# Kernel tuning notes

Hardware: AMD Instinct MI355X
Metric: run time of the kernel (lower is better)

## Reference

```python
import jax, jax.numpy as jnp
import numpy as np

N, MAX_SIZE, SPATIAL = 50000, 32, 27
CH_IN, CH_OUT = 128, 128


def setup_inputs() -> dict:
    key = jax.random.key(0)
    k1, k2, k3, k4 = jax.random.split(key, 4)
    feat_in = jax.random.normal(k1, (N, CH_IN), dtype=jnp.float32)
    select_mat = jax.random.uniform(k2, (N, MAX_SIZE, SPATIAL), dtype=jnp.float32)
    # kaiming-uniform-ish init for weight of shape [SPATIAL, CH_OUT*CH_IN]
    fan_in = CH_OUT * CH_IN
    bound = np.sqrt(6.0 / fan_in)
    weight = jax.random.uniform(k3, (SPATIAL, CH_OUT * CH_IN), dtype=jnp.float32,
                                minval=-bound, maxval=bound)
    neighbor_idx = jax.random.randint(k4, (N, MAX_SIZE), 0, N, dtype=jnp.int64)
    return {"feat_in": feat_in, "select_mat": select_mat,
            "weight": weight, "neighbor_idx": neighbor_idx}


def reference(feat_in, select_mat, weight, neighbor_idx):
    # feat_in: [N, I]; select_mat: [N, M, S]; weight: [S, O*I]; neighbor_idx: [N, M]
    ch_in = feat_in.shape[1]
    spatial = weight.shape[0]
    ch_out = weight.shape[1] // ch_in
    w = weight.reshape(spatial, ch_out, ch_in)          # [S, O, I]
    patch_feat = feat_in[neighbor_idx]                  # irregular gather -> [N, M, I]
    # Original math: out[n,o] = sum_m sum_s sel[n,m,s] * W[s,o,i] * pf[n,m,i]
    # Contract neighbor dim first to avoid the [N, M, O, I] intermediate.
    t = jnp.einsum('nms,nmi->nsi', select_mat, patch_feat)   # [N, S, I]
    feat_out = jnp.einsum('nsi,soi->no', t, w)               # [N, O]
    return feat_out[:, :, None]                              # [N, O, 1]
```

## Files before the change

### kernel.cpp

```cpp
#include <hip/hip_runtime.h>


#define N_CHI 128
#define N_SP  27
#define N_M   32
#define KDIM  (N_SP * N_CHI)
#define SEL_STRIDE (N_M * N_SP)

typedef short s16x8 __attribute__((ext_vector_type(8)));
typedef s16x8 __attribute__((may_alias)) s16x8_a;
typedef unsigned short u16x8 __attribute__((ext_vector_type(8)));
typedef u16x8 __attribute__((may_alias)) u16x8_a;
typedef unsigned short u16x4 __attribute__((ext_vector_type(4)));
typedef u16x4 __attribute__((may_alias)) u16x4_a;
typedef unsigned int u32x2 __attribute__((ext_vector_type(2)));
typedef u32x2 __attribute__((may_alias)) u32x2_a;
typedef float f32x4 __attribute__((ext_vector_type(4)));
typedef f32x4 __attribute__((may_alias)) f32x4_a;
typedef float f32x16 __attribute__((ext_vector_type(16)));

typedef __attribute__((address_space(3))) unsigned int as3_u32;
typedef __attribute__((address_space(1))) const unsigned int as1_u32;

static __device__ __forceinline__ unsigned short f2bf(float f) {
  unsigned int u = __float_as_uint(f);
  u += 0x7FFFu + ((u >> 16) & 1u);
  return (unsigned short)(u >> 16);
}

__global__ __launch_bounds__(128) void wconv_kernel(const float* __restrict__ w,
                                                    unsigned short* __restrict__ Wt) {
  const int s = blockIdx.x;
  const int o = blockIdx.y;
  const int i = threadIdx.x;
  Wt[((size_t)o * N_SP + s) * N_CHI + i] = f2bf(w[((size_t)s * 128 + o) * N_CHI + i]);
}

__global__ __launch_bounds__(256) void featconv_kernel(
    const float* __restrict__ feat, unsigned short* __restrict__ featb, int total4) {
  const int t = blockIdx.x * 256 + threadIdx.x;
  if (t < total4) {
    f32x4 v = ((const f32x4_a*)feat)[t];
    u16x4 o;
#pragma unroll
    for (int j = 0; j < 4; ++j) o[j] = f2bf(v[j]);
    ((u16x4_a*)featb)[t] = o;
  }
}

__global__ __launch_bounds__(256) void phase1_kernel(
    const unsigned short* __restrict__ featb, const float* __restrict__ sel,
    const int* __restrict__ nidx, unsigned short* __restrict__ T,
    int nbase, int nend) {
  __shared__ __align__(16) unsigned short selT[4][32 * 40];
  __shared__ __align__(16) unsigned short tbuf[4][N_SP * 128];
  const int wave = threadIdx.x >> 6;
  const int lane = threadIdx.x & 63;
  const int n = nbase + (int)blockIdx.x * 4 + wave;
  if (n >= nend) return;
  unsigned short* st = selT[wave];
  unsigned short* tb = tbuf[wave];

  const float* selp = sel + (size_t)n * SEL_STRIDE;
#pragma unroll
  for (int it = 0; it < 16; ++it) {
    int e = it * 64 + lane;
    int m = e >> 5, s = e & 31;
    float v = (s < N_SP) ? selp[m * N_SP + s] : 0.0f;
    st[s * 40 + m] = f2bf(v);
  }

  const int q = lane >> 5;
  const int col = lane & 31;

  const int* ip = nidx + (size_t)n * N_M;
  size_t roff[16];
#pragma unroll
  for (int ks = 0; ks < 2; ++ks)
#pragma unroll
    for (int j = 0; j < 8; ++j)
      roff[ks * 8 + j] = (size_t)ip[ks * 16 + q * 8 + j] << 7;

  const s16x8 bf0 = *(const s16x8_a*)&st[col * 40 + q * 8];
  const s16x8 bf1 = *(const s16x8_a*)&st[col * 40 + 16 + q * 8];

#pragma unroll
  for (int ti = 0; ti < 4; ++ti) {
    const int icol = ti * 32 + col;
    unsigned short fv[16];
#pragma unroll
    for (int t = 0; t < 16; ++t) fv[t] = featb[roff[t] + icol];
    s16x8 af0, af1;
#pragma unroll
    for (int j = 0; j < 8; ++j) {
      af0[j] = (short)fv[j];
      af1[j] = (short)fv[8 + j];
    }
    f32x16 acc = {0.f, 0.f, 0.f, 0.f, 0.f, 0.f, 0.f, 0.f,
                  0.f, 0.f, 0.f, 0.f, 0.f, 0.f, 0.f, 0.f};
    acc = __builtin_amdgcn_mfma_f32_32x32x16_bf16(af0, bf0, acc, 0, 0, 0);
    acc = __builtin_amdgcn_mfma_f32_32x32x16_bf16(af1, bf1, acc, 0, 0, 0);
    if (col < N_SP) {
#pragma unroll
      for (int g = 0; g < 4; ++g) {
        const int b16 = ti * 4 + g;
        const int phys16 = b16 ^ (col & 15);
        u32x2 pk;
        pk[0] = (unsigned int)f2bf(acc[4 * g + 0]) | ((unsigned int)f2bf(acc[4 * g + 1]) << 16);
        pk[1] = (unsigned int)f2bf(acc[4 * g + 2]) | ((unsigned int)f2bf(acc[4 * g + 3]) << 16);
        *(u32x2_a*)&tb[col * 128 + phys16 * 8 + q * 4] = pk;
      }
    }
  }

  unsigned short* Tn = T + (size_t)(n - nbase) * KDIM;
#pragma unroll
  for (int it = 0; it < 7; ++it) {
    const int P = it * 64 + lane;
    if (P < 432) {
      const int c = P >> 4;
      const int b16 = P & 15;
      const int phys16 = b16 ^ (c & 15);
      *(u16x8_a*)&Tn[(size_t)P * 8] = *(const u16x8_a*)&tb[c * 128 + phys16 * 8];
    }
  }
}

__global__ __launch_bounds__(256) void phase2_kernel(
    const unsigned short* __restrict__ T, const unsigned short* __restrict__ Wt,
    float* __restrict__ out, int nbase, int N) {
  __shared__ __align__(16) unsigned short Alds[64 * 128];
  __shared__ __align__(16) unsigned short Blds[128 * 128];
  const int tid = threadIdx.x;
  const int lane = tid & 63;
  const int wbase = tid & ~63;
  const int wave = tid >> 6;
  const int wm = wave & 1, wn = wave >> 1;
  const int quad = lane >> 4, l16 = lane & 15;
  const size_t rowbase = (size_t)blockIdx.x * 64;

  f32x4 acc[2][4];
#pragma unroll
  for (int a = 0; a < 2; ++a)
#pragma unroll
    for (int b = 0; b < 4; ++b) acc[a][b] = (f32x4){0.f, 0.f, 0.f, 0.f};

  const unsigned short* aga[4];
  const unsigned short* bga[8];
#pragma unroll
  for (int it = 0; it < 4; ++it) {
    const int slot = it * 256 + tid;
    const int r = slot >> 4, bp = slot & 15;
    aga[it] = T + (rowbase + r) * KDIM + ((bp ^ (r & 15)) << 3);
  }
#pragma unroll
  for (int it = 0; it < 8; ++it) {
    const int slot = it * 256 + tid;
    const int r = slot >> 4, bp = slot & 15;
    bga[it] = Wt + (size_t)r * KDIM + ((bp ^ (r & 15)) << 3);
  }

  for (int kt = 0; kt < KDIM / 128; ++kt) {
    const int k0 = kt * 128;
#pragma unroll
    for (int it = 0; it < 4; ++it)
      __builtin_amdgcn_global_load_lds(
          (as1_u32*)(const void*)(aga[it] + k0),
          (as3_u32*)(void*)&Alds[(it * 256 + wbase) * 8], 16, 0, 0);
#pragma unroll
    for (int it = 0; it < 8; ++it)
      __builtin_amdgcn_global_load_lds(
          (as1_u32*)(const void*)(bga[it] + k0),
          (as3_u32*)(void*)&Blds[(it * 256 + wbase) * 8], 16, 0, 0);
    __syncthreads();
#pragma unroll
    for (int ks = 0; ks < 4; ++ks) {
      const int bg = ks * 4 + quad;
      s16x8 af[2], bfr[4];
#pragma unroll
      for (int mt = 0; mt < 2; ++mt) {
        const int m = wm * 32 + mt * 16 + l16;
        af[mt] = *(const s16x8_a*)&Alds[m * 128 + ((bg ^ (m & 15)) << 3)];
      }
#pragma unroll
      for (int nt = 0; nt < 4; ++nt) {
        const int o = wn * 64 + nt * 16 + l16;
        bfr[nt] = *(const s16x8_a*)&Blds[o * 128 + ((bg ^ (o & 15)) << 3)];
      }
#pragma unroll
      for (int mt = 0; mt < 2; ++mt)
#pragma unroll
        for (int nt = 0; nt < 4; ++nt)
          acc[mt][nt] = __builtin_amdgcn_mfma_f32_16x16x32_bf16(af[mt], bfr[nt],
                                                                acc[mt][nt], 0, 0, 0);
    }
    __syncthreads();
  }

#pragma unroll
  for (int mt = 0; mt < 2; ++mt) {
    const int growb = nbase + (int)rowbase + wm * 32 + mt * 16 + quad * 4;
#pragma unroll
    for (int r = 0; r < 4; ++r) {
      const int grow = growb + r;
      if (grow < N) {
#pragma unroll
        for (int nt = 0; nt < 4; ++nt) {
          const int o = wn * 64 + nt * 16 + l16;
          out[(size_t)grow * 128 + o] = acc[mt][nt][r];
        }
      }
    }
  }
}

extern "C" void kernel_launch(void* const* d_in, const int* in_sizes, int n_in,
                              void* d_out, int out_size, void* d_ws, size_t ws_size,
                              hipStream_t stream) {
  const float* feat = (const float*)d_in[0];
  const float* sel  = (const float*)d_in[1];
  const float* wgt  = (const float*)d_in[2];
  const int*   nidx = (const int*)d_in[3];
  float* out = (float*)d_out;
  const int N = in_sizes[0] / N_CHI;
  const int total = in_sizes[0];

  unsigned short* Wt = (unsigned short*)d_ws;
  const size_t WT_ELEMS = (size_t)128 * KDIM;
  unsigned short* featb = Wt + WT_ELEMS;
  const size_t FB_ELEMS = (size_t)N * N_CHI;
  unsigned short* T = featb + FB_ELEMS;

  wconv_kernel<<<dim3(N_SP, 128), 128, 0, stream>>>(wgt, Wt);
  featconv_kernel<<<dim3((unsigned)((total / 4 + 255) / 256)), 256, 0, stream>>>(
      feat, featb, total / 4);

  const size_t head = (WT_ELEMS + FB_ELEMS) * 2;
  const size_t bytes_for_T = (ws_size > head) ? (ws_size - head) : 0;
  long cap_rows = (long)(bytes_for_T / ((size_t)KDIM * 2));
  long NC = (cap_rows / 64) * 64;
  const long Nfull = (((long)N + 63) / 64) * 64;
  if (NC > Nfull) NC = Nfull;
  if (NC <= 0) return;

  for (long nb = 0; nb < N; nb += NC) {
    long rows = (long)N - nb;
    if (rows > NC) rows = NC;
    const long rows64 = ((rows + 63) / 64) * 64;
    phase1_kernel<<<dim3((unsigned)((rows + 3) / 4)), 256, 0, stream>>>(
        featb, sel, nidx, T, (int)nb, (int)(nb + rows));
    phase2_kernel<<<dim3((unsigned)(rows64 / 64)), 256, 0, stream>>>(
        T, Wt, out, (int)nb, N);
  }
}
```

Baseline: 556.1 us.

## Load GEMM fragments directly from global and prefetch gathers in phase1

Phase2 drops the LDS-staged 64x128 tile GEMM in favour of per-wave 32-row tiles whose A and B MFMA fragments are loaded straight from global memory, with 128 rows per block. This removes the syncthreads barriers and LDS traffic, but B (the weights) is no longer shared through LDS, so each wave re-reads it from global/L2. Phase1 builds the select-matrix fragments directly in registers instead of transposing through LDS, and double-buffers the feature gather loads across the four column tiles. Chunk sizing is changed to 128-row granularity to match.

New measurement: 640.9 us. 15.3% more time.

```diff
diff --git a/kernel.cpp b/kernel.cpp
--- a/kernel.cpp
+++ b/kernel.cpp
@@ -19,9 +19,6 @@
 typedef f32x4 __attribute__((may_alias)) f32x4_a;
 typedef float f32x16 __attribute__((ext_vector_type(16)));
 
-typedef __attribute__((address_space(3))) unsigned int as3_u32;
-typedef __attribute__((address_space(1))) const unsigned int as1_u32;
-
 static __device__ __forceinline__ unsigned short f2bf(float f) {
   unsigned int u = __float_as_uint(f);
   u += 0x7FFFu + ((u >> 16) & 1u);
@@ -52,26 +49,26 @@
     const unsigned short* __restrict__ featb, const float* __restrict__ sel,
     const int* __restrict__ nidx, unsigned short* __restrict__ T,
     int nbase, int nend) {
-  __shared__ __align__(16) unsigned short selT[4][32 * 40];
   __shared__ __align__(16) unsigned short tbuf[4][N_SP * 128];
   const int wave = threadIdx.x >> 6;
   const int lane = threadIdx.x & 63;
   const int n = nbase + (int)blockIdx.x * 4 + wave;
   if (n >= nend) return;
-  unsigned short* st = selT[wave];
   unsigned short* tb = tbuf[wave];
-
-  const float* selp = sel + (size_t)n * SEL_STRIDE;
-#pragma unroll
-  for (int it = 0; it < 16; ++it) {
-    int e = it * 64 + lane;
-    int m = e >> 5, s = e & 31;
-    float v = (s < N_SP) ? selp[m * N_SP + s] : 0.0f;
-    st[s * 40 + m] = f2bf(v);
-  }
 
   const int q = lane >> 5;
   const int col = lane & 31;
+  const int colc = (col < N_SP) ? col : N_SP - 1;
+
+  const float* selp = sel + (size_t)n * SEL_STRIDE;
+  s16x8 bf0, bf1;
+#pragma unroll
+  for (int j = 0; j < 8; ++j) {
+    float v0 = selp[(q * 8 + j) * N_SP + colc];
+    float v1 = selp[(16 + q * 8 + j) * N_SP + colc];
+    bf0[j] = (short)((col < N_SP) ? f2bf(v0) : (unsigned short)0);
+    bf1[j] = (short)((col < N_SP) ? f2bf(v1) : (unsigned short)0);
+  }
 
   const int* ip = nidx + (size_t)n * N_M;
   size_t roff[16];
@@ -81,20 +78,22 @@
     for (int j = 0; j < 8; ++j)
       roff[ks * 8 + j] = (size_t)ip[ks * 16 + q * 8 + j] << 7;
 
-  const s16x8 bf0 = *(const s16x8_a*)&st[col * 40 + q * 8];
-  const s16x8 bf1 = *(const s16x8_a*)&st[col * 40 + 16 + q * 8];
-
+  unsigned short fv[2][16];
+#pragma unroll
+  for (int t = 0; t < 16; ++t) fv[0][t] = featb[roff[t] + col];
 #pragma unroll
   for (int ti = 0; ti < 4; ++ti) {
-    const int icol = ti * 32 + col;
-    unsigned short fv[16];
-#pragma unroll
-    for (int t = 0; t < 16; ++t) fv[t] = featb[roff[t] + icol];
+    const int cur = ti & 1;
+    if (ti < 3) {
+      const int icol = (ti + 1) * 32 + col;
+#pragma unroll
+      for (int t = 0; t < 16; ++t) fv[cur ^ 1][t] = featb[roff[t] + icol];
+    }
     s16x8 af0, af1;
 #pragma unroll
     for (int j = 0; j < 8; ++j) {
-      af0[j] = (short)fv[j];
-      af1[j] = (short)fv[8 + j];
+      af0[j] = (short)fv[cur][j];
+      af1[j] = (short)fv[cur][8 + j];
     }
     f32x16 acc = {0.f, 0.f, 0.f, 0.f, 0.f, 0.f, 0.f, 0.f,
                   0.f, 0.f, 0.f, 0.f, 0.f, 0.f, 0.f, 0.f};
@@ -129,86 +128,47 @@
 __global__ __launch_bounds__(256) void phase2_kernel(
     const unsigned short* __restrict__ T, const unsigned short* __restrict__ Wt,
     float* __restrict__ out, int nbase, int N) {
-  __shared__ __align__(16) unsigned short Alds[64 * 128];
-  __shared__ __align__(16) unsigned short Blds[128 * 128];
-  const int tid = threadIdx.x;
-  const int lane = tid & 63;
-  const int wbase = tid & ~63;
-  const int wave = tid >> 6;
-  const int wm = wave & 1, wn = wave >> 1;
-  const int quad = lane >> 4, l16 = lane & 15;
-  const size_t rowbase = (size_t)blockIdx.x * 64;
-
-  f32x4 acc[2][4];
-#pragma unroll
-  for (int a = 0; a < 2; ++a)
-#pragma unroll
-    for (int b = 0; b < 4; ++b) acc[a][b] = (f32x4){0.f, 0.f, 0.f, 0.f};
-
-  const unsigned short* aga[4];
-  const unsigned short* bga[8];
-#pragma unroll
-  for (int it = 0; it < 4; ++it) {
-    const int slot = it * 256 + tid;
-    const int r = slot >> 4, bp = slot & 15;
-    aga[it] = T + (rowbase + r) * KDIM + ((bp ^ (r & 15)) << 3);
-  }
-#pragma unroll
-  for (int it = 0; it < 8; ++it) {
-    const int slot = it * 256 + tid;
-    const int r = slot >> 4, bp = slot & 15;
-    bga[it] = Wt + (size_t)r * KDIM + ((bp ^ (r & 15)) << 3);
-  }
-
-  for (int kt = 0; kt < KDIM / 128; ++kt) {
-    const int k0 = kt * 128;
-#pragma unroll
-    for (int it = 0; it < 4; ++it)
-      __builtin_amdgcn_global_load_lds(
-          (as1_u32*)(const void*)(aga[it] + k0),
-          (as3_u32*)(void*)&Alds[(it * 256 + wbase) * 8], 16, 0, 0);
-#pragma unroll
-    for (int it = 0; it < 8; ++it)
-      __builtin_amdgcn_global_load_lds(
-          (as1_u32*)(const void*)(bga[it] + k0),
-          (as3_u32*)(void*)&Blds[(it * 256 + wbase) * 8], 16, 0, 0);
-    __syncthreads();
-#pragma unroll
-    for (int ks = 0; ks < 4; ++ks) {
-      const int bg = ks * 4 + quad;
-      s16x8 af[2], bfr[4];
-#pragma unroll
-      for (int mt = 0; mt < 2; ++mt) {
-        const int m = wm * 32 + mt * 16 + l16;
-        af[mt] = *(const s16x8_a*)&Alds[m * 128 + ((bg ^ (m & 15)) << 3)];
-      }
-#pragma unroll
-      for (int nt = 0; nt < 4; ++nt) {
-        const int o = wn * 64 + nt * 16 + l16;
-        bfr[nt] = *(const s16x8_a*)&Blds[o * 128 + ((bg ^ (o & 15)) << 3)];
-      }
-#pragma unroll
-      for (int mt = 0; mt < 2; ++mt)
-#pragma unroll
-        for (int nt = 0; nt < 4; ++nt)
-          acc[mt][nt] = __builtin_amdgcn_mfma_f32_16x16x32_bf16(af[mt], bfr[nt],
-                                                                acc[mt][nt], 0, 0, 0);
-    }
-    __syncthreads();
-  }
-
-#pragma unroll
-  for (int mt = 0; mt < 2; ++mt) {
-    const int growb = nbase + (int)rowbase + wm * 32 + mt * 16 + quad * 4;
+  const int lane = threadIdx.x & 63;
+  const int wave = threadIdx.x >> 6;
+  const int q = lane >> 4, l16 = lane & 15;
+  const size_t rb = (size_t)blockIdx.x * 128 + (size_t)wave * 32;
+
+  const unsigned short* a0 = T + (rb + l16) * KDIM + q * 8;
+  const unsigned short* a1 = a0 + (size_t)16 * KDIM;
+  const unsigned short* bp = Wt + (size_t)l16 * KDIM + q * 8;
+
+  f32x4 acc[2][8];
+#pragma unroll
+  for (int g = 0; g < 2; ++g)
+#pragma unroll
+    for (int nt = 0; nt < 8; ++nt) acc[g][nt] = (f32x4){0.f, 0.f, 0.f, 0.f};
+
+#pragma unroll 2
+  for (int kt = 0; kt < KDIM / 32; ++kt) {
+    const int k = kt * 32;
+    const s16x8 A0 = *(const s16x8_a*)(a0 + k);
+    const s16x8 A1 = *(const s16x8_a*)(a1 + k);
+    s16x8 B[8];
+#pragma unroll
+    for (int nt = 0; nt < 8; ++nt)
+      B[nt] = *(const s16x8_a*)(bp + (size_t)nt * 16 * KDIM + k);
+#pragma unroll
+    for (int nt = 0; nt < 8; ++nt) {
+      acc[0][nt] = __builtin_amdgcn_mfma_f32_16x16x32_bf16(A0, B[nt], acc[0][nt], 0, 0, 0);
+      acc[1][nt] = __builtin_amdgcn_mfma_f32_16x16x32_bf16(A1, B[nt], acc[1][nt], 0, 0, 0);
+    }
+  }
+
+#pragma unroll
+  for (int g = 0; g < 2; ++g) {
+    const long growb = (long)nbase + (long)rb + g * 16 + q * 4;
 #pragma unroll
     for (int r = 0; r < 4; ++r) {
-      const int grow = growb + r;
+      const long grow = growb + r;
       if (grow < N) {
 #pragma unroll
-        for (int nt = 0; nt < 4; ++nt) {
-          const int o = wn * 64 + nt * 16 + l16;
-          out[(size_t)grow * 128 + o] = acc[mt][nt][r];
-        }
+        for (int nt = 0; nt < 8; ++nt)
+          out[grow * 128 + nt * 16 + l16] = acc[g][nt][r];
       }
     }
   }
@@ -238,18 +198,18 @@
   const size_t head = (WT_ELEMS + FB_ELEMS) * 2;
   const size_t bytes_for_T = (ws_size > head) ? (ws_size - head) : 0;
   long cap_rows = (long)(bytes_for_T / ((size_t)KDIM * 2));
-  long NC = (cap_rows / 64) * 64;
-  const long Nfull = (((long)N + 63) / 64) * 64;
+  long NC = (cap_rows / 128) * 128;
+  const long Nfull = (((long)N + 127) / 128) * 128;
   if (NC > Nfull) NC = Nfull;
   if (NC <= 0) return;
 
   for (long nb = 0; nb < N; nb += NC) {
     long rows = (long)N - nb;
     if (rows > NC) rows = NC;
-    const long rows64 = ((rows + 63) / 64) * 64;
+    const long rows128 = ((rows + 127) / 128) * 128;
     phase1_kernel<<<dim3((unsigned)((rows + 3) / 4)), 256, 0, stream>>>(
         featb, sel, nidx, T, (int)nb, (int)(nb + rows));
-    phase2_kernel<<<dim3((unsigned)(rows64 / 64)), 256, 0, stream>>>(
+    phase2_kernel<<<dim3((unsigned)(rows128 / 128)), 256, 0, stream>>>(
         T, Wt, out, (int)nb, N);
   }
 }
```
